# Kernel optimization log

Measured on AMD Instinct MI355X. Metric: run time of the kernel, lower is better.

Reference implementation:

```python
import jax, jax.numpy as jnp
import numpy as np

N1, N2, D = 8192, 8192, 128

def setup_inputs() -> dict:
    key = jax.random.key(0)
    k1, k2 = jax.random.split(key)
    desc1 = jax.random.normal(k1, (N1, D), dtype=jnp.float32)
    desc2 = jax.random.normal(k2, (N2, D), dtype=jnp.float32)
    return {"desc1": desc1, "desc2": desc2}

def reference(desc1, desc2):
    # sim: [N1, N2] descriptor similarity matrix
    sim = desc1 @ desc2.T
    # mutual nearest-neighbor matching ('nnm' mode)
    nn12 = jnp.argmax(sim, axis=1)            # [N1] best match in image 2 for each kp in image 1
    nn21 = jnp.argmax(sim, axis=0)            # [N2] best match in image 1 for each kp in image 2
    ids1 = jnp.arange(sim.shape[0])
    mutual = nn21[nn12] == ids1               # mutual-consistency check
    # dense jit-friendly encoding of the ragged match list: -1 where no mutual match
    matches0 = jnp.where(mutual, nn12, -1)    # [N1] int
    # matching_scores0 = top-1 similarity per row (torch.topk(..., k=1)[0].squeeze())
    scores = jnp.max(sim, axis=1)             # [N1]
    return matches0, scores
```

## Files before the change

### kernel.cpp

```cpp
#include <hip/hip_runtime.h>
#include <stdint.h>

#define N1 8192
#define N2 8192
#define DK 128
#define TAU 0.08f
#define BIAS 256.0f
#define LDR 132

typedef _Float16 half8 __attribute__((ext_vector_type(8)));
typedef _Float16 half4 __attribute__((ext_vector_type(4)));
typedef float floatx4 __attribute__((ext_vector_type(4)));

__device__ __align__(16) _Float16 g_Af[N1 * DK];
__device__ __align__(16) _Float16 g_Bf[N2 * DK];
__device__ __align__(16) float2 g_rowtop2[64 * N1];
__device__ __align__(16) float2 g_coltop2[64 * N2];
__device__ int g_nn21[N2];

__device__ __forceinline__ float bkey(float v, unsigned idx) {
    unsigned b = __float_as_uint(v + BIAS);
    return __uint_as_float((b & 0xFFFFFF80u) | idx);
}
__device__ __forceinline__ float bval(float key) {
    return __uint_as_float(__float_as_uint(key) & 0xFFFFFF80u);
}
__device__ __forceinline__ int bidx(float key) {
    return (int)(__float_as_uint(key) & 127u);
}
__device__ __forceinline__ void push2f(float& t1, float& t2, float p) {
    float m = __builtin_amdgcn_fmed3f(t1, t2, p);
    t1 = fmaxf(t1, p);
    t2 = m;
}
__device__ __forceinline__ void merge2f(float& t1, float& t2, float o1, float o2) {
    float x = fmaxf(t2, o2);
    float m = __builtin_amdgcn_fmed3f(t1, o1, x);
    t1 = fmaxf(t1, o1);
    t2 = m;
}
__device__ __forceinline__ unsigned mono32(float v) {
    unsigned u = __float_as_uint(v);
    return u ^ ((u & 0x80000000u) ? 0xFFFFFFFFu : 0x80000000u);
}
__device__ __forceinline__ float unmono32(unsigned k) {
    unsigned u = (k & 0x80000000u) ? (k ^ 0x80000000u) : ~k;
    return __uint_as_float(u);
}
__device__ __forceinline__ unsigned long long pack64(float d, unsigned idx) {
    return ((unsigned long long)mono32(d) << 32) | (unsigned)(~idx);
}

__global__ __launch_bounds__(256) void convert_kernel(const float* __restrict__ A,
                                                      const float* __restrict__ B) {
    int t = blockIdx.x * blockDim.x + threadIdx.x;
    const int perMat = N1 * (DK / 4);
    int which = (t >= perMat) ? 1 : 0;
    const float* src = which ? B : A;
    _Float16* dst = which ? g_Bf : g_Af;
    int i = which ? t - perMat : t;
    int m = i >> 5;
    int kq = i & 31;
    float4 v = *reinterpret_cast<const float4*>(src + (size_t)m * DK + kq * 4);
    half4 h = {(_Float16)v.x, (_Float16)v.y, (_Float16)v.z, (_Float16)v.w};
    *reinterpret_cast<half4*>(dst + (size_t)m * DK + kq * 4) = h;
}

__global__ __launch_bounds__(256) void simf16_kernel() {
    __shared__ _Float16 As[128 * LDR];
    __shared__ _Float16 Bs[128 * LDR];
    __shared__ float2 lmerge[2][128];

    const int tid  = threadIdx.x;
    const int lane = tid & 63;
    const int wave = tid >> 6;
    const int wm = wave >> 1, wn = wave & 1;
    const int fr = lane & 15, q = lane >> 4;

    const int flat = blockIdx.y * 64 + blockIdx.x;
    const int xcd = flat & 7;
    const int j = flat >> 3;
    const int ty = j >> 3;
    const int tx = ((j & 7) << 3) | xcd;
    const int row0 = ty * 128, col0 = tx * 128;

#pragma unroll
    for (int i = 0; i < 8; ++i) {
        int f = i * 256 + tid;
        int r = f >> 4, c = f & 15;
        *reinterpret_cast<float4*>(&As[r * LDR + c * 8]) =
            *reinterpret_cast<const float4*>(g_Af + (size_t)(row0 + r) * DK + c * 8);
        *reinterpret_cast<float4*>(&Bs[r * LDR + c * 8]) =
            *reinterpret_cast<const float4*>(g_Bf + (size_t)(col0 + r) * DK + c * 8);
    }
    __syncthreads();

    floatx4 acc[4][4];
#pragma unroll
    for (int mt = 0; mt < 4; ++mt)
#pragma unroll
        for (int nt = 0; nt < 4; ++nt)
            acc[mt][nt] = (floatx4){0.f, 0.f, 0.f, 0.f};

#pragma unroll
    for (int ks = 0; ks < 4; ++ks) {
        half8 af[4], bf[4];
#pragma unroll
        for (int mt = 0; mt < 4; ++mt)
            af[mt] = *reinterpret_cast<const half8*>(&As[(wm * 64 + mt * 16 + fr) * LDR + ks * 32 + q * 8]);
#pragma unroll
        for (int nt = 0; nt < 4; ++nt)
            bf[nt] = *reinterpret_cast<const half8*>(&Bs[(wn * 64 + nt * 16 + fr) * LDR + ks * 32 + q * 8]);
#pragma unroll
        for (int mt = 0; mt < 4; ++mt)
#pragma unroll
            for (int nt = 0; nt < 4; ++nt)
                acc[mt][nt] = __builtin_amdgcn_mfma_f32_16x16x32_f16(af[mt], bf[nt], acc[mt][nt], 0, 0, 0);
    }

#pragma unroll
    for (int mt = 0; mt < 4; ++mt) {
#pragma unroll
        for (int reg = 0; reg < 4; ++reg) {
            float t1 = 0.f, t2 = 0.f;
#pragma unroll
            for (int nt = 0; nt < 4; ++nt)
                push2f(t1, t2, bkey(acc[mt][nt][reg], (unsigned)(wn * 64 + nt * 16 + fr)));
#pragma unroll
            for (int off = 1; off < 16; off <<= 1) {
                float o1 = __shfl_xor(t1, off, 64);
                float o2 = __shfl_xor(t2, off, 64);
                merge2f(t1, t2, o1, o2);
            }
            if (fr == 0) lmerge[wn][wm * 64 + mt * 16 + q * 4 + reg] = make_float2(t1, t2);
        }
    }
    __syncthreads();
    if (tid < 128) {
        float2 a = lmerge[0][tid], b = lmerge[1][tid];
        merge2f(a.x, a.y, b.x, b.y);
        g_rowtop2[(size_t)tx * N1 + row0 + tid] = a;
    }
    __syncthreads();

#pragma unroll
    for (int nt = 0; nt < 4; ++nt) {
        float t1 = 0.f, t2 = 0.f;
#pragma unroll
        for (int mt = 0; mt < 4; ++mt)
#pragma unroll
            for (int reg = 0; reg < 4; ++reg)
                push2f(t1, t2, bkey(acc[mt][nt][reg], (unsigned)(wm * 64 + mt * 16 + q * 4 + reg)));
        float o1 = __shfl_xor(t1, 16, 64), o2 = __shfl_xor(t2, 16, 64);
        merge2f(t1, t2, o1, o2);
        o1 = __shfl_xor(t1, 32, 64); o2 = __shfl_xor(t2, 32, 64);
        merge2f(t1, t2, o1, o2);
        if (q == 0) lmerge[wm][wn * 64 + nt * 16 + fr] = make_float2(t1, t2);
    }
    __syncthreads();
    if (tid < 128) {
        float2 a = lmerge[0][tid], b = lmerge[1][tid];
        merge2f(a.x, a.y, b.x, b.y);
        g_coltop2[(size_t)ty * N2 + col0 + tid] = a;
    }
}

__global__ __launch_bounds__(256) void colfix_kernel(const float* __restrict__ A,
                                                     const float* __restrict__ B) {
    __shared__ float2 tile[64 * 16];
    __shared__ unsigned long long slot[16];
    __shared__ int cand[256];
    __shared__ int cand_cnt;

    const int tid = threadIdx.x;
    const int c0 = blockIdx.x * 16;

#pragma unroll
    for (int i = 0; i < 4; ++i) {
        int idx = i * 256 + tid;
        int grp = idx >> 4, c = idx & 15;
        tile[grp * 16 + c] = g_coltop2[(size_t)grp * N2 + c0 + c];
    }
    if (tid < 16) slot[tid] = 0ULL;
    if (tid == 0) cand_cnt = 0;
    __syncthreads();

    const int c = tid >> 4, j = tid & 15;
    float mx = 0.f;
#pragma unroll
    for (int s = 0; s < 4; ++s)
        mx = fmaxf(mx, tile[(j * 4 + s) * 16 + c].x);
    mx = fmaxf(mx, __shfl_xor(mx, 1, 64));
    mx = fmaxf(mx, __shfl_xor(mx, 2, 64));
    mx = fmaxf(mx, __shfl_xor(mx, 4, 64));
    mx = fmaxf(mx, __shfl_xor(mx, 8, 64));
    const float thr = bval(mx) - TAU;
#pragma unroll
    for (int s = 0; s < 4; ++s) {
        int grp = j * 4 + s;
        float2 e = tile[grp * 16 + c];
        if (bval(e.x) >= thr) {
            int rr = grp * 128 + bidx(e.x);
            int si = atomicAdd(&cand_cnt, 1);
            if (si < 256) cand[si] = (c << 16) | rr;
        }
        if (bval(e.y) >= thr) {
            int rr = grp * 128 + bidx(e.y);
            int si = atomicAdd(&cand_cnt, 1);
            if (si < 256) cand[si] = (c << 16) | rr;
        }
    }
    __syncthreads();

    const int nc = min(cand_cnt, 256);
    for (int i = tid; i < nc; i += 256) {
        int pc = cand[i];
        int cl = pc >> 16, rr = pc & 0xFFFF;
        const float* ar = A + (size_t)rr * DK;
        const float* br = B + (size_t)(c0 + cl) * DK;
        float d = 0.0f;
#pragma unroll
        for (int k4 = 0; k4 < DK / 4; ++k4) {
            float4 a = *reinterpret_cast<const float4*>(ar + k4 * 4);
            float4 b = *reinterpret_cast<const float4*>(br + k4 * 4);
            d = fmaf(a.x, b.x, d);
            d = fmaf(a.y, b.y, d);
            d = fmaf(a.z, b.z, d);
            d = fmaf(a.w, b.w, d);
        }
        atomicMax(&slot[cl], pack64(d, (unsigned)rr));
    }
    __syncthreads();

    if (tid < 16) g_nn21[c0 + tid] = (int)(~(unsigned)slot[tid]);
}

__global__ __launch_bounds__(256) void rowfix_mutual_kernel(const float* __restrict__ A,
                                                            const float* __restrict__ B,
                                                            float* __restrict__ out) {
    __shared__ float2 tile[64 * 16];
    __shared__ unsigned long long slot[16];
    __shared__ int cand[256];
    __shared__ int cand_cnt;

    const int tid = threadIdx.x;
    const int r0 = blockIdx.x * 16;

#pragma unroll
    for (int i = 0; i < 4; ++i) {
        int idx = i * 256 + tid;
        int grp = idx >> 4, r = idx & 15;
        tile[grp * 16 + r] = g_rowtop2[(size_t)grp * N1 + r0 + r];
    }
    if (tid < 16) slot[tid] = 0ULL;
    if (tid == 0) cand_cnt = 0;
    __syncthreads();

    const int r = tid >> 4, j = tid & 15;
    float mx = 0.f;
#pragma unroll
    for (int s = 0; s < 4; ++s)
        mx = fmaxf(mx, tile[(j * 4 + s) * 16 + r].x);
    mx = fmaxf(mx, __shfl_xor(mx, 1, 64));
    mx = fmaxf(mx, __shfl_xor(mx, 2, 64));
    mx = fmaxf(mx, __shfl_xor(mx, 4, 64));
    mx = fmaxf(mx, __shfl_xor(mx, 8, 64));
    const float thr = bval(mx) - TAU;
#pragma unroll
    for (int s = 0; s < 4; ++s) {
        int grp = j * 4 + s;
        float2 e = tile[grp * 16 + r];
        if (bval(e.x) >= thr) {
            int cc = grp * 128 + bidx(e.x);
            int si = atomicAdd(&cand_cnt, 1);
            if (si < 256) cand[si] = (r << 16) | cc;
        }
        if (bval(e.y) >= thr) {
            int cc = grp * 128 + bidx(e.y);
            int si = atomicAdd(&cand_cnt, 1);
            if (si < 256) cand[si] = (r << 16) | cc;
        }
    }
    __syncthreads();

    const int nc = min(cand_cnt, 256);
    for (int i = tid; i < nc; i += 256) {
        int pc = cand[i];
        int rl = pc >> 16, cc = pc & 0xFFFF;
        const float* ar = A + (size_t)(r0 + rl) * DK;
        const float* br = B + (size_t)cc * DK;
        float d = 0.0f;
#pragma unroll
        for (int k4 = 0; k4 < DK / 4; ++k4) {
            float4 a = *reinterpret_cast<const float4*>(ar + k4 * 4);
            float4 b = *reinterpret_cast<const float4*>(br + k4 * 4);
            d = fmaf(a.x, b.x, d);
            d = fmaf(a.y, b.y, d);
            d = fmaf(a.z, b.z, d);
            d = fmaf(a.w, b.w, d);
        }
        atomicMax(&slot[rl], pack64(d, (unsigned)cc));
    }
    __syncthreads();

    if (tid < 16) {
        unsigned long long p = slot[tid];
        int row = r0 + tid;
        int m = (int)(~(unsigned)p);
        out[row] = (float)((g_nn21[m] == row) ? m : -1);
        out[N1 + row] = unmono32((unsigned)(p >> 32));
    }
}

extern "C" void kernel_launch(void* const* d_in, const int* in_sizes, int n_in,
                              void* d_out, int out_size, void* d_ws, size_t ws_size,
                              hipStream_t stream) {
    const float* A = (const float*)d_in[0];
    const float* B = (const float*)d_in[1];
    float* out = (float*)d_out;

    convert_kernel<<<2 * N1 * (DK / 4) / 256, 256, 0, stream>>>(A, B);
    dim3 grid(64, 64);
    simf16_kernel<<<grid, 256, 0, stream>>>();
    colfix_kernel<<<N2 / 16, 256, 0, stream>>>(A, B);
    rowfix_mutual_kernel<<<N1 / 16, 256, 0, stream>>>(A, B, out);
}
```

Baseline: 137.6 us.

## Fuse fp16 conversion into GEMM tile load and merge row/col fixup kernels

Drops the separate convert kernel. The sim kernel now reads fp32 A/B directly and converts each tile to fp16 with packed round-toward-zero converts while staging into shared memory. The column and row fixup kernels become one 1024-block launch, followed by a small mutual-check kernel. This removes an intermediate fp16 buffer round trip and one launch, and lets both fixup halves run concurrently. In exchange, each sim block reads twice the global bytes (fp32 instead of fp16), and the rounding mode changes from round-to-nearest to round-toward-zero.

```diff
diff --git a/kernel.cpp b/kernel.cpp
--- a/kernel.cpp
+++ b/kernel.cpp
@@ -9,13 +9,12 @@
 #define LDR 132
 
 typedef _Float16 half8 __attribute__((ext_vector_type(8)));
-typedef _Float16 half4 __attribute__((ext_vector_type(4)));
+typedef __fp16 fp16x2 __attribute__((ext_vector_type(2)));
 typedef float floatx4 __attribute__((ext_vector_type(4)));
 
-__device__ __align__(16) _Float16 g_Af[N1 * DK];
-__device__ __align__(16) _Float16 g_Bf[N2 * DK];
 __device__ __align__(16) float2 g_rowtop2[64 * N1];
 __device__ __align__(16) float2 g_coltop2[64 * N2];
+__device__ int g_nn12[N1];
 __device__ int g_nn21[N2];
 
 __device__ __forceinline__ float bkey(float v, unsigned idx) {
@@ -50,23 +49,18 @@
 __device__ __forceinline__ unsigned long long pack64(float d, unsigned idx) {
     return ((unsigned long long)mono32(d) << 32) | (unsigned)(~idx);
 }
-
-__global__ __launch_bounds__(256) void convert_kernel(const float* __restrict__ A,
-                                                      const float* __restrict__ B) {
-    int t = blockIdx.x * blockDim.x + threadIdx.x;
-    const int perMat = N1 * (DK / 4);
-    int which = (t >= perMat) ? 1 : 0;
-    const float* src = which ? B : A;
-    _Float16* dst = which ? g_Bf : g_Af;
-    int i = which ? t - perMat : t;
-    int m = i >> 5;
-    int kq = i & 31;
-    float4 v = *reinterpret_cast<const float4*>(src + (size_t)m * DK + kq * 4);
-    half4 h = {(_Float16)v.x, (_Float16)v.y, (_Float16)v.z, (_Float16)v.w};
-    *reinterpret_cast<half4*>(dst + (size_t)m * DK + kq * 4) = h;
-}
-
-__global__ __launch_bounds__(256) void simf16_kernel() {
+__device__ __forceinline__ half8 cvt8(float4 lo, float4 hi) {
+    fp16x2 p0 = __builtin_amdgcn_cvt_pkrtz(lo.x, lo.y);
+    fp16x2 p1 = __builtin_amdgcn_cvt_pkrtz(lo.z, lo.w);
+    fp16x2 p2 = __builtin_amdgcn_cvt_pkrtz(hi.x, hi.y);
+    fp16x2 p3 = __builtin_amdgcn_cvt_pkrtz(hi.z, hi.w);
+    union { fp16x2 h2[4]; half8 h8; } u;
+    u.h2[0] = p0; u.h2[1] = p1; u.h2[2] = p2; u.h2[3] = p3;
+    return u.h8;
+}
+
+__global__ __launch_bounds__(256) void simf16_kernel(const float* __restrict__ A,
+                                                     const float* __restrict__ B) {
     __shared__ _Float16 As[128 * LDR];
     __shared__ _Float16 Bs[128 * LDR];
     __shared__ float2 lmerge[2][128];
@@ -88,10 +82,14 @@
     for (int i = 0; i < 8; ++i) {
         int f = i * 256 + tid;
         int r = f >> 4, c = f & 15;
-        *reinterpret_cast<float4*>(&As[r * LDR + c * 8]) =
-            *reinterpret_cast<const float4*>(g_Af + (size_t)(row0 + r) * DK + c * 8);
-        *reinterpret_cast<float4*>(&Bs[r * LDR + c * 8]) =
-            *reinterpret_cast<const float4*>(g_Bf + (size_t)(col0 + r) * DK + c * 8);
+        const float* pa = A + (size_t)(row0 + r) * DK + c * 8;
+        const float* pb = B + (size_t)(col0 + r) * DK + c * 8;
+        *reinterpret_cast<half8*>(&As[r * LDR + c * 8]) =
+            cvt8(*reinterpret_cast<const float4*>(pa),
+                 *reinterpret_cast<const float4*>(pa + 4));
+        *reinterpret_cast<half8*>(&Bs[r * LDR + c * 8]) =
+            cvt8(*reinterpret_cast<const float4*>(pb),
+                 *reinterpret_cast<const float4*>(pb + 4));
     }
     __syncthreads();
 
@@ -165,21 +163,24 @@
     }
 }
 
-__global__ __launch_bounds__(256) void colfix_kernel(const float* __restrict__ A,
-                                                     const float* __restrict__ B) {
+__global__ __launch_bounds__(256) void fix_kernel(const float* __restrict__ A,
+                                                  const float* __restrict__ B,
+                                                  float* __restrict__ out) {
     __shared__ float2 tile[64 * 16];
     __shared__ unsigned long long slot[16];
     __shared__ int cand[256];
     __shared__ int cand_cnt;
 
     const int tid = threadIdx.x;
-    const int c0 = blockIdx.x * 16;
+    const bool rowside = blockIdx.x >= 512;
+    const int base0 = (blockIdx.x & 511) * 16;
+    const float2* top2 = rowside ? g_rowtop2 : g_coltop2;
 
 #pragma unroll
     for (int i = 0; i < 4; ++i) {
         int idx = i * 256 + tid;
         int grp = idx >> 4, c = idx & 15;
-        tile[grp * 16 + c] = g_coltop2[(size_t)grp * N2 + c0 + c];
+        tile[grp * 16 + c] = top2[(size_t)grp * N1 + base0 + c];
     }
     if (tid < 16) slot[tid] = 0ULL;
     if (tid == 0) cand_cnt = 0;
@@ -200,14 +201,14 @@
         int grp = j * 4 + s;
         float2 e = tile[grp * 16 + c];
         if (bval(e.x) >= thr) {
-            int rr = grp * 128 + bidx(e.x);
+            int o = grp * 128 + bidx(e.x);
             int si = atomicAdd(&cand_cnt, 1);
-            if (si < 256) cand[si] = (c << 16) | rr;
+            if (si < 256) cand[si] = (c << 16) | o;
         }
         if (bval(e.y) >= thr) {
-            int rr = grp * 128 + bidx(e.y);
+            int o = grp * 128 + bidx(e.y);
             int si = atomicAdd(&cand_cnt, 1);
-            if (si < 256) cand[si] = (c << 16) | rr;
+            if (si < 256) cand[si] = (c << 16) | o;
         }
     }
     __syncthreads();
@@ -215,9 +216,9 @@
     const int nc = min(cand_cnt, 256);
     for (int i = tid; i < nc; i += 256) {
         int pc = cand[i];
-        int cl = pc >> 16, rr = pc & 0xFFFF;
-        const float* ar = A + (size_t)rr * DK;
-        const float* br = B + (size_t)(c0 + cl) * DK;
+        int cl = pc >> 16, other = pc & 0xFFFF;
+        const float* ar = rowside ? (A + (size_t)(base0 + cl) * DK) : (A + (size_t)other * DK);
+        const float* br = rowside ? (B + (size_t)other * DK) : (B + (size_t)(base0 + cl) * DK);
         float d = 0.0f;
 #pragma unroll
         for (int k4 = 0; k4 < DK / 4; ++k4) {
@@ -228,87 +229,27 @@
             d = fmaf(a.z, b.z, d);
             d = fmaf(a.w, b.w, d);
         }
-        atomicMax(&slot[cl], pack64(d, (unsigned)rr));
-    }
-    __syncthreads();
-
-    if (tid < 16) g_nn21[c0 + tid] = (int)(~(unsigned)slot[tid]);
-}
-
-__global__ __launch_bounds__(256) void rowfix_mutual_kernel(const float* __restrict__ A,
-                                                            const float* __restrict__ B,
-                                                            float* __restrict__ out) {
-    __shared__ float2 tile[64 * 16];
-    __shared__ unsigned long long slot[16];
-    __shared__ int cand[256];
-    __shared__ int cand_cnt;
-
-    const int tid = threadIdx.x;
-    const int r0 = blockIdx.x * 16;
-
-#pragma unroll
-    for (int i = 0; i < 4; ++i) {
-        int idx = i * 256 + tid;
-        int grp = idx >> 4, r = idx & 15;
-        tile[grp * 16 + r] = g_rowtop2[(size_t)grp * N1 + r0 + r];
-    }
-    if (tid < 16) slot[tid] = 0ULL;
-    if (tid == 0) cand_cnt = 0;
-    __syncthreads();
-
-    const int r = tid >> 4, j = tid & 15;
-    float mx = 0.f;
-#pragma unroll
-    for (int s = 0; s < 4; ++s)
-        mx = fmaxf(mx, tile[(j * 4 + s) * 16 + r].x);
-    mx = fmaxf(mx, __shfl_xor(mx, 1, 64));
-    mx = fmaxf(mx, __shfl_xor(mx, 2, 64));
-    mx = fmaxf(mx, __shfl_xor(mx, 4, 64));
-    mx = fmaxf(mx, __shfl_xor(mx, 8, 64));
-    const float thr = bval(mx) - TAU;
-#pragma unroll
-    for (int s = 0; s < 4; ++s) {
-        int grp = j * 4 + s;
-        float2 e = tile[grp * 16 + r];
-        if (bval(e.x) >= thr) {
-            int cc = grp * 128 + bidx(e.x);
-            int si = atomicAdd(&cand_cnt, 1);
-            if (si < 256) cand[si] = (r << 16) | cc;
-        }
-        if (bval(e.y) >= thr) {
-            int cc = grp * 128 + bidx(e.y);
-            int si = atomicAdd(&cand_cnt, 1);
-            if (si < 256) cand[si] = (r << 16) | cc;
-        }
-    }
-    __syncthreads();
-
-    const int nc = min(cand_cnt, 256);
-    for (int i = tid; i < nc; i += 256) {
-        int pc = cand[i];
-        int rl = pc >> 16, cc = pc & 0xFFFF;
-        const float* ar = A + (size_t)(r0 + rl) * DK;
-        const float* br = B + (size_t)cc * DK;
-        float d = 0.0f;
-#pragma unroll
-        for (int k4 = 0; k4 < DK / 4; ++k4) {
-            float4 a = *reinterpret_cast<const float4*>(ar + k4 * 4);
-            float4 b = *reinterpret_cast<const float4*>(br + k4 * 4);
-            d = fmaf(a.x, b.x, d);
-            d = fmaf(a.y, b.y, d);
-            d = fmaf(a.z, b.z, d);
-            d = fmaf(a.w, b.w, d);
-        }
-        atomicMax(&slot[rl], pack64(d, (unsigned)cc));
+        atomicMax(&slot[cl], pack64(d, (unsigned)other));
     }
     __syncthreads();
 
     if (tid < 16) {
         unsigned long long p = slot[tid];
-        int row = r0 + tid;
-        int m = (int)(~(unsigned)p);
-        out[row] = (float)((g_nn21[m] == row) ? m : -1);
-        out[N1 + row] = unmono32((unsigned)(p >> 32));
+        int idx = base0 + tid;
+        if (rowside) {
+            g_nn12[idx] = (int)(~(unsigned)p);
+            out[N1 + idx] = unmono32((unsigned)(p >> 32));
+        } else {
+            g_nn21[idx] = (int)(~(unsigned)p);
+        }
+    }
+}
+
+__global__ __launch_bounds__(256) void mutual_kernel(float* __restrict__ out) {
+    int i = blockIdx.x * blockDim.x + threadIdx.x;
+    if (i < N1) {
+        int m = g_nn12[i];
+        out[i] = (float)((g_nn21[m] == i) ? m : -1);
     }
 }
 
@@ -319,9 +260,8 @@
     const float* B = (const float*)d_in[1];
     float* out = (float*)d_out;
 
-    convert_kernel<<<2 * N1 * (DK / 4) / 256, 256, 0, stream>>>(A, B);
     dim3 grid(64, 64);
-    simf16_kernel<<<grid, 256, 0, stream>>>();
-    colfix_kernel<<<N2 / 16, 256, 0, stream>>>(A, B);
-    rowfix_mutual_kernel<<<N1 / 16, 256, 0, stream>>>(A, B, out);
-}
+    simf16_kernel<<<grid, 256, 0, stream>>>(A, B);
+    fix_kernel<<<1024, 256, 0, stream>>>(A, B, out);
+    mutual_kernel<<<N1 / 256, 256, 0, stream>>>(out);
+}
```

Result: no change. 136.6 us (-0.7%).
